# Kernel tuning notes

Measured on AMD Instinct MI355X. Metric: run time of the kernel, lower is better.

The kernel has to match this reference:

```python
import jax, jax.numpy as jnp
import numpy as np

# Production-scale perfect decision-tree ensemble (Hummingbird perf_tree_trav layout)
B, F, T, D, C = 16384, 256, 512, 7, 4  # batch, features, trees, internal levels below root, classes


def setup_inputs() -> dict:
    key = jax.random.key(0)
    k = jax.random.split(key, 6)
    total = T * (2 ** (D + 1) - 2)  # concatenated per-level node/bias tables, level l has T*2^l entries
    return {
        "x": jax.random.normal(k[0], (B, F), dtype=jnp.float32),
        "root_nodes": jax.random.randint(k[1], (T,), 0, F, dtype=jnp.int32),
        "root_biases": jax.random.normal(k[2], (T,), dtype=jnp.float32),
        "tree_indices": jnp.arange(T, dtype=jnp.int32) * 2,
        "nodes_flat": jax.random.randint(k[3], (total,), 0, F, dtype=jnp.int32),
        "biases_flat": jax.random.normal(k[4], (total,), dtype=jnp.float32),
        "leaf_nodes": jax.random.normal(k[5], (T * 2 ** (D + 1), C), dtype=jnp.float32),
    }


def reference(x, root_nodes, root_biases, tree_indices, nodes_flat, biases_flat, leaf_nodes):
    # Root level: compare each tree's root feature against its bias. decision_cond = less (lt).
    # tree_indices = t*2 offsets indices into the flat level-1 table of size 2T;
    # the offset doubles along with the level size via `2*idx + cond`.
    idx = (x[:, root_nodes] < root_biases).astype(jnp.int32) + tree_indices  # [B, T]
    off = 0
    for l in range(1, D + 1):  # static loop over tree depth
        size = T << l
        lvl_nodes = nodes_flat[off:off + size]
        lvl_biases = biases_flat[off:off + size]
        feat_idx = lvl_nodes[idx]                          # [B, T] feature ids for current nodes
        feats = jnp.take_along_axis(x, feat_idx, axis=1)   # [B, T] per-sample feature gather
        idx = 2 * idx + (feats < lvl_biases[idx]).astype(jnp.int32)
        off += size
    leaves = leaf_nodes[idx]                               # [B, T, C]
    return leaves.sum(axis=1)                              # [B, C]
```

## Files before the change

### kernel.cpp

```cpp
#include <hip/hip_runtime.h>
#include <hip/hip_fp16.h>

#define BB 16384
#define FF 256
#define TT 512
#define DD 7

constexpr int S_  = 64;
constexpr int NT_ = 1024;
constexpr int NTG = NT_ / S_;
constexpr int HT  = TT / 2;
constexpr int TPT = HT / NTG;
constexpr int NP  = 8;
constexpr int NJ  = TPT / NP;

constexpr int NR1 = TT * 2;
constexpr int NR3 = TT * 8;
constexpr int NR5 = TT * 32;
constexpr int NN7 = TT * 128;
constexpr int NTOT = NR1 + NR3 + NR5 + NN7 + NN7;

constexpr size_t OFF_R3   = (size_t)NR1 * 16;
constexpr size_t OFF_R5   = OFF_R3 + (size_t)NR3 * 16;
constexpr size_t OFF_N7   = OFF_R5 + (size_t)NR5 * 16;
constexpr size_t OFF_LP   = OFF_N7 + (size_t)NN7 * 8;
constexpr size_t OFF_PART = OFF_LP + (size_t)NN7 * 16;
constexpr size_t WS_NEED  = OFF_PART + (size_t)2 * BB * 4 * sizeof(float);

__global__ void pack_kernel(const int* __restrict__ nf, const float* __restrict__ bf,
                            const float4* __restrict__ leaf4,
                            int4* __restrict__ R1, int4* __restrict__ R3,
                            int4* __restrict__ R5, int2* __restrict__ N7,
                            uint4* __restrict__ LP) {
    const int i = blockIdx.x * 256 + threadIdx.x;
    if (i < NR1) {
        const int e0 = i, eC = 2 * TT + 2 * i;
        const int fp = (nf[e0] & 255) | ((nf[eC] & 255) << 8) | ((nf[eC + 1] & 255) << 16);
        R1[i] = make_int4(fp, __float_as_int(bf[e0]),
                          __float_as_int(bf[eC]), __float_as_int(bf[eC + 1]));
    } else if (i < NR1 + NR3) {
        const int r = i - NR1;
        const int e0 = 6 * TT + r, eC = 14 * TT + 2 * r;
        const int fp = (nf[e0] & 255) | ((nf[eC] & 255) << 8) | ((nf[eC + 1] & 255) << 16);
        R3[r] = make_int4(fp, __float_as_int(bf[e0]),
                          __float_as_int(bf[eC]), __float_as_int(bf[eC + 1]));
    } else if (i < NR1 + NR3 + NR5) {
        const int r = i - NR1 - NR3;
        const int e0 = 30 * TT + r, eC = 62 * TT + 2 * r;
        const int fp = (nf[e0] & 255) | ((nf[eC] & 255) << 8) | ((nf[eC + 1] & 255) << 16);
        R5[r] = make_int4(fp, __float_as_int(bf[e0]),
                          __float_as_int(bf[eC]), __float_as_int(bf[eC + 1]));
    } else if (i < NR1 + NR3 + NR5 + NN7) {
        const int r = i - NR1 - NR3 - NR5;
        const int e = 126 * TT + r;
        N7[r] = make_int2(nf[e] & 255, __float_as_int(bf[e]));
    } else if (i < NTOT) {
        const int j = i - NR1 - NR3 - NR5 - NN7;
        const float4 l0 = leaf4[2 * j], l1 = leaf4[2 * j + 1];
        const __half2 a = __floats2half2_rn(l0.x, l0.y), b = __floats2half2_rn(l0.z, l0.w);
        const __half2 c = __floats2half2_rn(l1.x, l1.y), d = __floats2half2_rn(l1.z, l1.w);
        uint4 w;
        w.x = *reinterpret_cast<const unsigned int*>(&a);
        w.y = *reinterpret_cast<const unsigned int*>(&b);
        w.z = *reinterpret_cast<const unsigned int*>(&c);
        w.w = *reinterpret_cast<const unsigned int*>(&d);
        LP[j] = w;
    }
}

__device__ __forceinline__ int step2(const int4 w, const int i,
                                     const float* __restrict__ x_s,
                                     const int xb, const int sz) {
    const float v0 = x_s[xb | ((w.x & 255) ^ sz)];
    const int   c0 = (v0 < __int_as_float(w.y)) ? 1 : 0;
    const int   fc = c0 ? ((w.x >> 16) & 255) : ((w.x >> 8) & 255);
    const float bc = c0 ? __int_as_float(w.w) : __int_as_float(w.z);
    const float vc = x_s[xb | (fc ^ sz)];
    const int   c1 = (vc < bc) ? 1 : 0;
    return 4 * i + 2 * c0 + c1;
}

__global__ __launch_bounds__(NT_, 8)
void tree_traverse_kernel(const float* __restrict__ x,
                          const int*   __restrict__ root_nodes,
                          const float* __restrict__ root_biases,
                          const int4*  __restrict__ R1, const int4* __restrict__ R3,
                          const int4*  __restrict__ R5, const int2* __restrict__ N7,
                          const uint4* __restrict__ LP,
                          float*       __restrict__ part)
{
    extern __shared__ float x_s[];

    const int tid = threadIdx.x;
    const int s   = tid & (S_ - 1);
    const int tg  = tid >> 6;
    const int s0  = blockIdx.x * S_;
    const int h0  = blockIdx.y * HT;

    {
        const float4* xg = (const float4*)(x + (size_t)s0 * FF);
        const int r  = tid >> 4;
        const int v  = tid & 15;
        const int rz = r & 31;
        float* row = x_s + (r << 8);
        #pragma unroll
        for (int c = 0; c < 4; ++c) {
            const float4 q = xg[r * (FF / 4) + v + 16 * c];
            const int f0 = (v + 16 * c) * 4;
            row[(f0 + 0) ^ rz] = q.x;
            row[(f0 + 1) ^ rz] = q.y;
            row[(f0 + 2) ^ rz] = q.z;
            row[(f0 + 3) ^ rz] = q.w;
        }
    }
    __syncthreads();

    const int xb = s << 8;
    const int sz = s & 31;
    float a0 = 0.f, a1 = 0.f, a2 = 0.f, a3 = 0.f;

    #pragma unroll 1
    for (int j = 0; j < NJ; ++j) {
        const int tbase = h0 + tg * TPT + j * NP;
        int p[NP];

        #pragma unroll
        for (int k = 0; k < NP; ++k) {
            const int tu = __builtin_amdgcn_readfirstlane(tbase + k);
            const int   rn  = root_nodes[tu];
            const float rbv = root_biases[tu];
            const int4  rA  = R1[2 * tu];
            const int4  rB  = R1[2 * tu + 1];
            const int c0 = (x_s[xb | (rn ^ sz)] < rbv) ? 1 : 0;
            int4 r;
            r.x = c0 ? rB.x : rA.x;  r.y = c0 ? rB.y : rA.y;
            r.z = c0 ? rB.z : rA.z;  r.w = c0 ? rB.w : rA.w;
            p[k] = step2(r, c0, x_s, xb, sz);
        }
        #pragma unroll
        for (int k = 0; k < NP; ++k)
            p[k] = step2(R3[((tbase + k) << 3) + p[k]], p[k], x_s, xb, sz);
        #pragma unroll
        for (int k = 0; k < NP; ++k)
            p[k] = step2(R5[((tbase + k) << 5) + p[k]], p[k], x_s, xb, sz);
        #pragma unroll
        for (int k = 0; k < NP; ++k) {
            const int idx7 = ((tbase + k) << 7) + p[k];
            const int2  n  = N7[idx7];
            const uint4 lp = LP[idx7];
            const int c7 = (x_s[xb | (n.x ^ sz)] < __int_as_float(n.y)) ? 1 : 0;
            const unsigned int w01 = c7 ? lp.z : lp.x;
            const unsigned int w23 = c7 ? lp.w : lp.y;
            const float2 f01 = __half22float2(*reinterpret_cast<const __half2*>(&w01));
            const float2 f23 = __half22float2(*reinterpret_cast<const __half2*>(&w23));
            a0 += f01.x; a1 += f01.y; a2 += f23.x; a3 += f23.y;
        }
    }

    __syncthreads();
    ((float4*)x_s)[tid] = make_float4(a0, a1, a2, a3);
    __syncthreads();
    if (tid < S_ * 4) {
        float o = 0.f;
        #pragma unroll
        for (int g = 0; g < NTG; ++g)
            o += x_s[(g << 8) + tid];
        part[((size_t)blockIdx.y * BB + s0) * 4 + tid] = o;
    }
}

__global__ void sum_kernel(const float4* __restrict__ part, float4* __restrict__ out) {
    const int i = blockIdx.x * 256 + threadIdx.x;
    if (i < BB) {
        const float4 a = part[i], b = part[BB + i];
        out[i] = make_float4(a.x + b.x, a.y + b.y, a.z + b.z, a.w + b.w);
    }
}

__global__ __launch_bounds__(NT_, 4)
void tree_traverse_fallback(const float* __restrict__ x,
                            const int* __restrict__ root_nodes,
                            const float* __restrict__ root_biases,
                            const int* __restrict__ nodes_flat,
                            const float* __restrict__ biases_flat,
                            const float* __restrict__ leaf_nodes,
                            float* __restrict__ out)
{
    extern __shared__ float x_s[];
    const int tid = threadIdx.x;
    const int s = tid & (S_ - 1), tg = tid >> 6;
    const int s0 = blockIdx.x * S_;
    {
        const float4* xg = (const float4*)(x + (size_t)s0 * FF);
        const int r = tid >> 4, v = tid & 15, rz = r & 31;
        float* row = x_s + (r << 8);
        #pragma unroll
        for (int c = 0; c < 4; ++c) {
            const float4 q = xg[r * (FF / 4) + v + 16 * c];
            const int f0 = (v + 16 * c) * 4;
            row[(f0 + 0) ^ rz] = q.x; row[(f0 + 1) ^ rz] = q.y;
            row[(f0 + 2) ^ rz] = q.z; row[(f0 + 3) ^ rz] = q.w;
        }
    }
    __syncthreads();
    const int xb = s << 8, sz = s & 31;
    const float4* leaf4 = (const float4*)leaf_nodes;
    float a0 = 0.f, a1 = 0.f, a2 = 0.f, a3 = 0.f;
    #pragma unroll 1
    for (int j = 0; j < TT / NTG / NP; ++j) {
        const int tbase = tg * (TT / NTG) + j * NP;
        int p[NP];
        #pragma unroll
        for (int k = 0; k < NP; ++k) {
            const int t = tbase + k;
            p[k] = 2 * t + ((x_s[xb | (root_nodes[t] ^ sz)] < root_biases[t]) ? 1 : 0);
        }
        #pragma unroll
        for (int l = 1; l <= DD; ++l) {
            #pragma unroll
            for (int k = 0; k < NP; ++k) {
                const int fi = nodes_flat[p[k]];
                const float bi = biases_flat[p[k]];
                const int c = (x_s[xb | (fi ^ sz)] < bi) ? 1 : 0;
                p[k] = 2 * p[k] + 2 * TT + c;
            }
        }
        #pragma unroll
        for (int k = 0; k < NP; ++k) {
            const float4 lf = leaf4[p[k] - 254 * TT];
            a0 += lf.x; a1 += lf.y; a2 += lf.z; a3 += lf.w;
        }
    }
    __syncthreads();
    ((float4*)x_s)[tid] = make_float4(a0, a1, a2, a3);
    __syncthreads();
    if (tid < S_ * 4) {
        float o = 0.f;
        #pragma unroll
        for (int g = 0; g < NTG; ++g) o += x_s[(g << 8) + tid];
        out[(size_t)s0 * 4 + tid] = o;
    }
}

extern "C" void kernel_launch(void* const* d_in, const int* in_sizes, int n_in,
                              void* d_out, int out_size, void* d_ws, size_t ws_size,
                              hipStream_t stream) {
    const float* x           = (const float*)d_in[0];
    const int*   root_nodes  = (const int*)  d_in[1];
    const float* root_biases = (const float*)d_in[2];
    const int*   nodes_flat  = (const int*)  d_in[4];
    const float* biases_flat = (const float*)d_in[5];
    const float* leaf_nodes  = (const float*)d_in[6];
    float*       out         = (float*)d_out;

    constexpr size_t LDS_BYTES = (size_t)S_ * FF * sizeof(float);

    if (ws_size >= WS_NEED) {
        char* ws = (char*)d_ws;
        int4*  R1 = (int4*)ws;
        int4*  R3 = (int4*)(ws + OFF_R3);
        int4*  R5 = (int4*)(ws + OFF_R5);
        int2*  N7 = (int2*)(ws + OFF_N7);
        uint4* LP = (uint4*)(ws + OFF_LP);
        float* part = (float*)(ws + OFF_PART);

        pack_kernel<<<(NTOT + 255) / 256, 256, 0, stream>>>(
            nodes_flat, biases_flat, (const float4*)leaf_nodes, R1, R3, R5, N7, LP);
        dim3 grid(BB / S_, 2);
        tree_traverse_kernel<<<grid, NT_, LDS_BYTES, stream>>>(
            x, root_nodes, root_biases, R1, R3, R5, N7, LP, part);
        sum_kernel<<<BB / 256, 256, 0, stream>>>((const float4*)part, (float4*)out);
    } else {
        tree_traverse_fallback<<<BB / S_, NT_, LDS_BYTES, stream>>>(
            x, root_nodes, root_biases, nodes_flat, biases_flat, leaf_nodes, out);
    }
}
```

Measured before the change: 103.0 us.

## Stage level-3/4 node table in LDS and process all trees per block

Adds a variant kernel that copies the packed level-3/4 node table (64 KB) into shared memory next to the 64 KB feature tile, and lets each block traverse all 512 trees, so the second grid dimension and the partial-sum reduction kernel go away. The aim is to move the R3 gathers from global/L2 to LDS and save one kernel launch. In exchange each block uses 128 KB of LDS, which lowers occupancy, and every block repeats the table copy. The host queries the device's shared memory per CU and falls back to the old two-pass path if 128 KB is not available.

```diff
diff --git a/kernel.cpp b/kernel.cpp
--- a/kernel.cpp
+++ b/kernel.cpp
@@ -5,14 +5,6 @@
 #define FF 256
 #define TT 512
 #define DD 7
-
-constexpr int S_  = 64;
-constexpr int NT_ = 1024;
-constexpr int NTG = NT_ / S_;
-constexpr int HT  = TT / 2;
-constexpr int TPT = HT / NTG;
-constexpr int NP  = 8;
-constexpr int NJ  = TPT / NP;
 
 constexpr int NR1 = TT * 2;
 constexpr int NR3 = TT * 8;
@@ -80,22 +72,23 @@
     return 4 * i + 2 * c0 + c1;
 }
 
-__global__ __launch_bounds__(NT_, 8)
-void tree_traverse_kernel(const float* __restrict__ x,
-                          const int*   __restrict__ root_nodes,
-                          const float* __restrict__ root_biases,
-                          const int4*  __restrict__ R1, const int4* __restrict__ R3,
-                          const int4*  __restrict__ R5, const int2* __restrict__ N7,
-                          const uint4* __restrict__ LP,
-                          float*       __restrict__ part)
+__global__ __launch_bounds__(1024, 4)
+void tree_traverse_big(const float* __restrict__ x,
+                       const int*   __restrict__ root_nodes,
+                       const float* __restrict__ root_biases,
+                       const int4*  __restrict__ R1, const int4* __restrict__ R3g,
+                       const int4*  __restrict__ R5, const int2* __restrict__ N7,
+                       const uint4* __restrict__ LP,
+                       float*       __restrict__ out)
 {
-    extern __shared__ float x_s[];
+    extern __shared__ float smem[];
+    float* x_s = smem;
+    int4*  r3s = (int4*)(smem + 16384);
 
     const int tid = threadIdx.x;
-    const int s   = tid & (S_ - 1);
+    const int s   = tid & 63;
     const int tg  = tid >> 6;
-    const int s0  = blockIdx.x * S_;
-    const int h0  = blockIdx.y * HT;
+    const int s0  = blockIdx.x * 64;
 
     {
         const float4* xg = (const float4*)(x + (size_t)s0 * FF);
@@ -112,6 +105,9 @@
             row[(f0 + 2) ^ rz] = q.z;
             row[(f0 + 3) ^ rz] = q.w;
         }
+        #pragma unroll
+        for (int i = 0; i < NR3 / 1024; ++i)
+            r3s[tid + i * 1024] = R3g[tid + i * 1024];
     }
     __syncthreads();
 
@@ -119,9 +115,13 @@
     const int sz = s & 31;
     float a0 = 0.f, a1 = 0.f, a2 = 0.f, a3 = 0.f;
 
+    constexpr int TPT = TT / 16;
+    constexpr int NP  = 8;
+    constexpr int NJ  = TPT / NP;
+
     #pragma unroll 1
     for (int j = 0; j < NJ; ++j) {
-        const int tbase = h0 + tg * TPT + j * NP;
+        const int tbase = tg * TPT + j * NP;
         int p[NP];
 
         #pragma unroll
@@ -139,7 +139,7 @@
         }
         #pragma unroll
         for (int k = 0; k < NP; ++k)
-            p[k] = step2(R3[((tbase + k) << 3) + p[k]], p[k], x_s, xb, sz);
+            p[k] = step2(r3s[((tbase + k) << 3) + p[k]], p[k], x_s, xb, sz);
         #pragma unroll
         for (int k = 0; k < NP; ++k)
             p[k] = step2(R5[((tbase + k) << 5) + p[k]], p[k], x_s, xb, sz);
@@ -160,10 +160,89 @@
     __syncthreads();
     ((float4*)x_s)[tid] = make_float4(a0, a1, a2, a3);
     __syncthreads();
-    if (tid < S_ * 4) {
+    if (tid < 256) {
         float o = 0.f;
         #pragma unroll
-        for (int g = 0; g < NTG; ++g)
+        for (int g = 0; g < 16; ++g)
+            o += x_s[(g << 8) + tid];
+        out[(size_t)s0 * 4 + tid] = o;
+    }
+}
+
+__global__ __launch_bounds__(1024, 8)
+void tree_traverse_kernel(const float* __restrict__ x,
+                          const int*   __restrict__ root_nodes,
+                          const float* __restrict__ root_biases,
+                          const int4*  __restrict__ R1, const int4* __restrict__ R3,
+                          const int4*  __restrict__ R5, const int2* __restrict__ N7,
+                          const uint4* __restrict__ LP,
+                          float*       __restrict__ part)
+{
+    extern __shared__ float x_s[];
+    const int tid = threadIdx.x;
+    const int s   = tid & 63;
+    const int tg  = tid >> 6;
+    const int s0  = blockIdx.x * 64;
+    const int h0  = blockIdx.y * (TT / 2);
+    {
+        const float4* xg = (const float4*)(x + (size_t)s0 * FF);
+        const int r = tid >> 4, v = tid & 15, rz = r & 31;
+        float* row = x_s + (r << 8);
+        #pragma unroll
+        for (int c = 0; c < 4; ++c) {
+            const float4 q = xg[r * (FF / 4) + v + 16 * c];
+            const int f0 = (v + 16 * c) * 4;
+            row[(f0 + 0) ^ rz] = q.x; row[(f0 + 1) ^ rz] = q.y;
+            row[(f0 + 2) ^ rz] = q.z; row[(f0 + 3) ^ rz] = q.w;
+        }
+    }
+    __syncthreads();
+    const int xb = s << 8, sz = s & 31;
+    float a0 = 0.f, a1 = 0.f, a2 = 0.f, a3 = 0.f;
+    constexpr int TPT = (TT / 2) / 16, NP = 8, NJ = TPT / NP;
+    #pragma unroll 1
+    for (int j = 0; j < NJ; ++j) {
+        const int tbase = h0 + tg * TPT + j * NP;
+        int p[NP];
+        #pragma unroll
+        for (int k = 0; k < NP; ++k) {
+            const int tu = __builtin_amdgcn_readfirstlane(tbase + k);
+            const int   rn  = root_nodes[tu];
+            const float rbv = root_biases[tu];
+            const int4  rA  = R1[2 * tu];
+            const int4  rB  = R1[2 * tu + 1];
+            const int c0 = (x_s[xb | (rn ^ sz)] < rbv) ? 1 : 0;
+            int4 r;
+            r.x = c0 ? rB.x : rA.x;  r.y = c0 ? rB.y : rA.y;
+            r.z = c0 ? rB.z : rA.z;  r.w = c0 ? rB.w : rA.w;
+            p[k] = step2(r, c0, x_s, xb, sz);
+        }
+        #pragma unroll
+        for (int k = 0; k < NP; ++k)
+            p[k] = step2(R3[((tbase + k) << 3) + p[k]], p[k], x_s, xb, sz);
+        #pragma unroll
+        for (int k = 0; k < NP; ++k)
+            p[k] = step2(R5[((tbase + k) << 5) + p[k]], p[k], x_s, xb, sz);
+        #pragma unroll
+        for (int k = 0; k < NP; ++k) {
+            const int idx7 = ((tbase + k) << 7) + p[k];
+            const int2  n  = N7[idx7];
+            const uint4 lp = LP[idx7];
+            const int c7 = (x_s[xb | (n.x ^ sz)] < __int_as_float(n.y)) ? 1 : 0;
+            const unsigned int w01 = c7 ? lp.z : lp.x;
+            const unsigned int w23 = c7 ? lp.w : lp.y;
+            const float2 f01 = __half22float2(*reinterpret_cast<const __half2*>(&w01));
+            const float2 f23 = __half22float2(*reinterpret_cast<const __half2*>(&w23));
+            a0 += f01.x; a1 += f01.y; a2 += f23.x; a3 += f23.y;
+        }
+    }
+    __syncthreads();
+    ((float4*)x_s)[tid] = make_float4(a0, a1, a2, a3);
+    __syncthreads();
+    if (tid < 256) {
+        float o = 0.f;
+        #pragma unroll
+        for (int g = 0; g < 16; ++g)
             o += x_s[(g << 8) + tid];
         part[((size_t)blockIdx.y * BB + s0) * 4 + tid] = o;
     }
@@ -177,7 +256,7 @@
     }
 }
 
-__global__ __launch_bounds__(NT_, 4)
+__global__ __launch_bounds__(1024, 4)
 void tree_traverse_fallback(const float* __restrict__ x,
                             const int* __restrict__ root_nodes,
                             const float* __restrict__ root_biases,
@@ -188,8 +267,8 @@
 {
     extern __shared__ float x_s[];
     const int tid = threadIdx.x;
-    const int s = tid & (S_ - 1), tg = tid >> 6;
-    const int s0 = blockIdx.x * S_;
+    const int s = tid & 63, tg = tid >> 6;
+    const int s0 = blockIdx.x * 64;
     {
         const float4* xg = (const float4*)(x + (size_t)s0 * FF);
         const int r = tid >> 4, v = tid & 15, rz = r & 31;
@@ -207,18 +286,18 @@
     const float4* leaf4 = (const float4*)leaf_nodes;
     float a0 = 0.f, a1 = 0.f, a2 = 0.f, a3 = 0.f;
     #pragma unroll 1
-    for (int j = 0; j < TT / NTG / NP; ++j) {
-        const int tbase = tg * (TT / NTG) + j * NP;
-        int p[NP];
-        #pragma unroll
-        for (int k = 0; k < NP; ++k) {
+    for (int j = 0; j < 4; ++j) {
+        const int tbase = tg * 32 + j * 8;
+        int p[8];
+        #pragma unroll
+        for (int k = 0; k < 8; ++k) {
             const int t = tbase + k;
             p[k] = 2 * t + ((x_s[xb | (root_nodes[t] ^ sz)] < root_biases[t]) ? 1 : 0);
         }
         #pragma unroll
         for (int l = 1; l <= DD; ++l) {
             #pragma unroll
-            for (int k = 0; k < NP; ++k) {
+            for (int k = 0; k < 8; ++k) {
                 const int fi = nodes_flat[p[k]];
                 const float bi = biases_flat[p[k]];
                 const int c = (x_s[xb | (fi ^ sz)] < bi) ? 1 : 0;
@@ -226,7 +305,7 @@
             }
         }
         #pragma unroll
-        for (int k = 0; k < NP; ++k) {
+        for (int k = 0; k < 8; ++k) {
             const float4 lf = leaf4[p[k] - 254 * TT];
             a0 += lf.x; a1 += lf.y; a2 += lf.z; a3 += lf.w;
         }
@@ -234,10 +313,10 @@
     __syncthreads();
     ((float4*)x_s)[tid] = make_float4(a0, a1, a2, a3);
     __syncthreads();
-    if (tid < S_ * 4) {
+    if (tid < 256) {
         float o = 0.f;
         #pragma unroll
-        for (int g = 0; g < NTG; ++g) o += x_s[(g << 8) + tid];
+        for (int g = 0; g < 16; ++g) o += x_s[(g << 8) + tid];
         out[(size_t)s0 * 4 + tid] = o;
     }
 }
@@ -253,7 +332,8 @@
     const float* leaf_nodes  = (const float*)d_in[6];
     float*       out         = (float*)d_out;
 
-    constexpr size_t LDS_BYTES = (size_t)S_ * FF * sizeof(float);
+    constexpr size_t LDS_SMALL = 65536;
+    constexpr size_t LDS_BIG   = 131072;
 
     if (ws_size >= WS_NEED) {
         char* ws = (char*)d_ws;
@@ -266,12 +346,31 @@
 
         pack_kernel<<<(NTOT + 255) / 256, 256, 0, stream>>>(
             nodes_flat, biases_flat, (const float4*)leaf_nodes, R1, R3, R5, N7, LP);
-        dim3 grid(BB / S_, 2);
-        tree_traverse_kernel<<<grid, NT_, LDS_BYTES, stream>>>(
-            x, root_nodes, root_biases, R1, R3, R5, N7, LP, part);
-        sum_kernel<<<BB / 256, 256, 0, stream>>>((const float4*)part, (float4*)out);
+
+        int dev = 0;
+        (void)hipGetDevice(&dev);
+        int smCU = 0;
+        (void)hipDeviceGetAttribute(&smCU,
+                hipDeviceAttributeMaxSharedMemoryPerMultiprocessor, dev);
+        bool big = false;
+        if (smCU >= (int)LDS_BIG) {
+            big = (hipFuncSetAttribute(
+                       reinterpret_cast<const void*>(&tree_traverse_big),
+                       hipFuncAttributeMaxDynamicSharedMemorySize,
+                       (int)LDS_BIG) == hipSuccess);
+        }
+
+        if (big) {
+            tree_traverse_big<<<BB / 64, 1024, LDS_BIG, stream>>>(
+                x, root_nodes, root_biases, R1, R3, R5, N7, LP, out);
+        } else {
+            dim3 grid(BB / 64, 2);
+            tree_traverse_kernel<<<grid, 1024, LDS_SMALL, stream>>>(
+                x, root_nodes, root_biases, R1, R3, R5, N7, LP, part);
+            sum_kernel<<<BB / 256, 256, 0, stream>>>((const float4*)part, (float4*)out);
+        }
     } else {
-        tree_traverse_fallback<<<BB / S_, NT_, LDS_BYTES, stream>>>(
+        tree_traverse_fallback<<<BB / 64, 1024, LDS_SMALL, stream>>>(
             x, root_nodes, root_biases, nodes_flat, biases_flat, leaf_nodes, out);
     }
 }
```

Result: no change. 103.5 us (+0.5%).
